# Kernel tuning notes

Measured on AMD Instinct MI355X. Metric: run time of the kernel, lower is better.

## Reference

```python
import jax, jax.numpy as jnp
import numpy as np

N_NODES = 50000
N_EDGES = 1_600_000
D_IN = 256
D_OUT = 256
BATCH = 4


def setup_inputs() -> dict:
    key = jax.random.key(0)
    k1, k2, k3, k4, k5, k6 = jax.random.split(key, 6)
    batch_input = jax.random.normal(k1, (BATCH, N_NODES, D_IN), dtype=jnp.float32)
    adj_rows = jax.random.randint(k2, (N_EDGES,), 0, N_NODES, dtype=jnp.int32)
    adj_cols = jax.random.randint(k3, (N_EDGES,), 0, N_NODES, dtype=jnp.int32)
    adj_vals = jax.random.uniform(k4, (N_EDGES,), dtype=jnp.float32)
    stdv = 1.0 / np.sqrt(D_OUT)
    weight = jax.random.uniform(k5, (D_IN, D_OUT), dtype=jnp.float32, minval=-stdv, maxval=stdv)
    b = jax.random.uniform(k6, (D_OUT,), dtype=jnp.float32, minval=-stdv, maxval=stdv)
    return {"batch_input": batch_input, "adj_rows": adj_rows, "adj_cols": adj_cols,
            "adj_vals": adj_vals, "weight": weight, "b": b}


def reference(batch_input, adj_rows, adj_cols, adj_vals, weight, b):
    # dense projection: [B, N, D_in] @ [D_in, D_out]
    support = jnp.einsum('bnf,fo->bno', batch_input, weight)

    # spmm with COO adjacency: out[r] = sum_e vals[e] * support[cols[e]] for rows[e]==r
    def spmm(s):  # s: [N, D_out]
        msgs = adj_vals[:, None] * s[adj_cols]          # [E, D_out]
        return jax.ops.segment_sum(msgs, adj_rows, num_segments=N_NODES)

    out = jax.vmap(spmm)(support)                       # [B, N, D_out]
    return out + b
```

## Files before the change

### kernel.cpp

```cpp
#include <hip/hip_runtime.h>

#define N_NODES 50000
#define D_DIM   256
#define N_BATCH 4
#define M_TOTAL (N_BATCH * N_NODES)

typedef __attribute__((ext_vector_type(8))) short bf16x8;
typedef __attribute__((ext_vector_type(4))) float f32x4;

__device__ inline float4 fma4(float a, float4 b, float4 c) {
    c.x = fmaf(a, b.x, c.x);
    c.y = fmaf(a, b.y, c.y);
    c.z = fmaf(a, b.z, c.z);
    c.w = fmaf(a, b.w, c.w);
    return c;
}

__device__ inline unsigned short f2bf(float f) {
    unsigned u = __float_as_uint(f);
    u = (u + 0x7fffu + ((u >> 16) & 1u)) >> 16;
    return (unsigned short)u;
}

__device__ inline float4 bf4tof4(ushort4 v) {
    return make_float4(__uint_as_float((unsigned)v.x << 16),
                       __uint_as_float((unsigned)v.y << 16),
                       __uint_as_float((unsigned)v.z << 16),
                       __uint_as_float((unsigned)v.w << 16));
}

__device__ inline int2 nt_edge(const int2* p) {
    long long raw = __builtin_nontemporal_load((const long long*)p);
    int2 r;
    r.x = (int)(unsigned long long)raw;
    r.y = (int)((unsigned long long)raw >> 32);
    return r;
}

__device__ inline void async_copy16(const unsigned short* g, unsigned short* l) {
    __builtin_amdgcn_global_load_lds(
        (const __attribute__((address_space(1))) char*)g,
        (__attribute__((address_space(3))) char*)l, 16, 0, 0);
}

__global__ void zero_kernel(int* __restrict__ p, int n) {
    int i = blockIdx.x * 256 + threadIdx.x;
    if (i < n) p[i] = 0;
}

__global__ void hist_kernel(const int* __restrict__ rows, int* __restrict__ counts, int E) {
    int e = blockIdx.x * 256 + threadIdx.x;
    if (e < E) atomicAdd(&counts[rows[e]], 1);
}

__global__ void scan_kernel(const int* __restrict__ counts, int* __restrict__ starts,
                            int* __restrict__ cursor, int n) {
    __shared__ int wsum[16];
    __shared__ int btot;
    const int tid  = threadIdx.x;
    const int lane = tid & 63;
    const int wid  = tid >> 6;
    int carry = 0;
    for (int base = 0; base < n; base += 1024) {
        int i = base + tid;
        int v = (i < n) ? counts[i] : 0;
        int x = v;
        #pragma unroll
        for (int s = 1; s < 64; s <<= 1) {
            int y = __shfl_up(x, s, 64);
            if (lane >= s) x += y;
        }
        if (lane == 63) wsum[wid] = x;
        __syncthreads();
        if (wid == 0 && lane < 16) {
            int w  = wsum[lane];
            int xx = w;
            #pragma unroll
            for (int s = 1; s < 16; s <<= 1) {
                int y = __shfl_up(xx, s, 64);
                if (lane >= s) xx += y;
            }
            wsum[lane] = xx - w;
            if (lane == 15) btot = xx;
        }
        __syncthreads();
        int excl = carry + wsum[wid] + x - v;
        if (i < n) { starts[i] = excl; cursor[i] = excl; }
        carry += btot;
        __syncthreads();
    }
    if (tid == 0) starts[n] = carry;
}

__global__ void scatter_kernel(const int* __restrict__ rows, const int* __restrict__ cols,
                               const float* __restrict__ vals, int* __restrict__ cursor,
                               int2* __restrict__ csr, int E) {
    int e = blockIdx.x * 256 + threadIdx.x;
    if (e < E) {
        int r   = rows[e];
        int pos = atomicAdd(&cursor[r], 1);
        csr[pos] = make_int2(cols[e], __float_as_int(vals[e]));
    }
}

__global__ void cast_x_kernel(const float4* __restrict__ X, ushort4* __restrict__ Xb, int n4) {
    int i = blockIdx.x * 256 + threadIdx.x;
    if (i < n4) {
        f32x4 v = __builtin_nontemporal_load((const f32x4*)&X[i]);
        ushort4 o;
        o.x = f2bf(v.x); o.y = f2bf(v.y); o.z = f2bf(v.z); o.w = f2bf(v.w);
        Xb[i] = o;
    }
}

__global__ void cast_wt_kernel(const float* __restrict__ W, unsigned short* __restrict__ Wt) {
    int i = blockIdx.x * 256 + threadIdx.x;
    int n = i >> 8, k = i & 255;
    Wt[n * 256 + k] = f2bf(W[k * 256 + n]);
}

__global__ __launch_bounds__(256) void gemm_mfma_kernel(const unsigned short* __restrict__ Xb,
                                                        const unsigned short* __restrict__ Wt,
                                                        unsigned short* __restrict__ sup) {
    __shared__ unsigned short at[128 * 32];
    __shared__ unsigned short bt[128 * 32];
    const int tid  = threadIdx.x;
    const int lane = tid & 63;
    const int wid  = tid >> 6;
    const int wm   = wid & 1, wn = wid >> 1;
    const int row0 = (blockIdx.x >> 1) * 128;
    const int col0 = (blockIdx.x & 1) * 128;
    const int fr    = lane & 15;
    const int fk    = (lane >> 4) * 8;
    const int srow  = lane >> 2;
    const int skoff = (lane & 3) * 8;

    f32x4 acc[4][4];
    #pragma unroll
    for (int a = 0; a < 4; ++a)
        #pragma unroll
        for (int b = 0; b < 4; ++b) acc[a][b] = (f32x4){0.f, 0.f, 0.f, 0.f};

    for (int kc = 0; kc < 256; kc += 32) {
        #pragma unroll
        for (int c = 0; c < 2; ++c) {
            int r = wid * 32 + c * 16;
            int gra = row0 + r + srow; if (gra >= M_TOTAL) gra = M_TOTAL - 1;
            async_copy16(Xb + (size_t)gra * 256 + kc + skoff, &at[r * 32]);
            int grb = col0 + r + srow;
            async_copy16(Wt + (size_t)grb * 256 + kc + skoff, &bt[r * 32]);
        }
        __syncthreads();
        bf16x8 af[4], bfr[4];
        #pragma unroll
        for (int t = 0; t < 4; ++t) {
            af[t]  = *(const bf16x8*)&at[(wm * 64 + t * 16 + fr) * 32 + fk];
            bfr[t] = *(const bf16x8*)&bt[(wn * 64 + t * 16 + fr) * 32 + fk];
        }
        #pragma unroll
        for (int tn = 0; tn < 4; ++tn)
            #pragma unroll
            for (int tm = 0; tm < 4; ++tm)
                acc[tn][tm] = __builtin_amdgcn_mfma_f32_16x16x32_bf16(bfr[tn], af[tm], acc[tn][tm], 0, 0, 0);
        __syncthreads();
    }

    #pragma unroll
    for (int tm = 0; tm < 4; ++tm) {
        int gr = row0 + wm * 64 + tm * 16 + fr;
        if (gr < M_TOTAL) {
            int b    = (int)((unsigned)gr / (unsigned)N_NODES);
            int node = gr - b * N_NODES;
            size_t base = ((size_t)node * 4 + b) * 256;
            #pragma unroll
            for (int tn = 0; tn < 4; ++tn) {
                int col = col0 + wn * 64 + tn * 16 + (lane >> 4) * 4;
                ushort4 o;
                o.x = f2bf(acc[tn][tm][0]);
                o.y = f2bf(acc[tn][tm][1]);
                o.z = f2bf(acc[tn][tm][2]);
                o.w = f2bf(acc[tn][tm][3]);
                *(ushort4*)&sup[base + col] = o;
            }
        }
    }
}

__global__ __launch_bounds__(256) void spmm_kernel(const unsigned short* __restrict__ sup,
                                                   const int* __restrict__ starts,
                                                   const int2* __restrict__ csr,
                                                   const float* __restrict__ bias,
                                                   float* __restrict__ out) {
    const int row  = blockIdx.x;
    const int b    = threadIdx.x >> 6;
    const int lane = threadIdx.x & 63;
    const unsigned short* supb = sup + (size_t)b * 256 + (size_t)lane * 4;
    const int s = starts[row];
    const int e = starts[row + 1];
    float4 acc = make_float4(0.f, 0.f, 0.f, 0.f);
    int i = s;
    for (; i + 7 < e; i += 8) {
        int2 ed[8];
        #pragma unroll
        for (int u = 0; u < 8; ++u) ed[u] = nt_edge(&csr[i + u]);
        ushort4 v[8];
        #pragma unroll
        for (int u = 0; u < 8; ++u) v[u] = *(const ushort4*)(supb + (size_t)ed[u].x * 1024);
        #pragma unroll
        for (int u = 0; u < 8; ++u) acc = fma4(__int_as_float(ed[u].y), bf4tof4(v[u]), acc);
    }
    for (; i + 1 < e; i += 2) {
        int2 e0 = nt_edge(&csr[i]);
        int2 e1 = nt_edge(&csr[i + 1]);
        ushort4 v0 = *(const ushort4*)(supb + (size_t)e0.x * 1024);
        ushort4 v1 = *(const ushort4*)(supb + (size_t)e1.x * 1024);
        acc = fma4(__int_as_float(e0.y), bf4tof4(v0), acc);
        acc = fma4(__int_as_float(e1.y), bf4tof4(v1), acc);
    }
    for (; i < e; ++i) {
        int2 e0 = nt_edge(&csr[i]);
        ushort4 v0 = *(const ushort4*)(supb + (size_t)e0.x * 1024);
        acc = fma4(__int_as_float(e0.y), bf4tof4(v0), acc);
    }
    float4 bb = ((const float4*)bias)[lane];
    f32x4 o;
    o.x = acc.x + bb.x; o.y = acc.y + bb.y; o.z = acc.z + bb.z; o.w = acc.w + bb.w;
    f32x4* dst = (f32x4*)out + ((size_t)b * N_NODES + row) * (D_DIM / 4) + lane;
    __builtin_nontemporal_store(o, dst);
}

extern "C" void kernel_launch(void* const* d_in, const int* in_sizes, int n_in,
                              void* d_out, int out_size, void* d_ws, size_t ws_size,
                              hipStream_t stream) {
    const float* X    = (const float*)d_in[0];
    const int*   rows = (const int*)d_in[1];
    const int*   cols = (const int*)d_in[2];
    const float* vals = (const float*)d_in[3];
    const float* W    = (const float*)d_in[4];
    const float* bias = (const float*)d_in[5];
    float*       out  = (float*)d_out;
    const int E = in_sizes[1];

    char* wsb = (char*)d_ws;
    size_t o = 0;
    auto alloc = [&](size_t bytes) -> char* {
        char* p = wsb + o;
        o += (bytes + 255) & ~(size_t)255;
        return p;
    };
    int*  counts = (int*)alloc((size_t)N_NODES * 4);
    int*  starts = (int*)alloc((size_t)(N_NODES + 1) * 4);
    int*  cursor = (int*)alloc((size_t)N_NODES * 4);
    int2* csr    = (int2*)alloc((size_t)E * 8);
    unsigned short* Xb  = (unsigned short*)alloc((size_t)M_TOTAL * D_DIM * 2);
    unsigned short* sup = (unsigned short*)alloc((size_t)N_NODES * N_BATCH * D_DIM * 2);
    unsigned short* Wt  = (unsigned short*)cursor;

    zero_kernel<<<(N_NODES + 255) / 256, 256, 0, stream>>>(counts, N_NODES);
    hist_kernel<<<(E + 255) / 256, 256, 0, stream>>>(rows, counts, E);
    scan_kernel<<<1, 1024, 0, stream>>>(counts, starts, cursor, N_NODES);
    scatter_kernel<<<(E + 255) / 256, 256, 0, stream>>>(rows, cols, vals, cursor, csr, E);

    const int n4 = M_TOTAL * D_DIM / 4;
    cast_x_kernel<<<(n4 + 255) / 256, 256, 0, stream>>>((const float4*)X, (ushort4*)Xb, n4);
    cast_wt_kernel<<<(256 * 256) / 256, 256, 0, stream>>>(W, Wt);

    const int rowTiles = (M_TOTAL + 127) / 128;
    gemm_mfma_kernel<<<rowTiles * 2, 256, 0, stream>>>(Xb, Wt, sup);

    spmm_kernel<<<N_NODES, 256, 0, stream>>>(sup, starts, csr, bias, out);
}
```

Measured before the change: 1.061 ms.

## Fuse X cast into GEMM, parallelize scan, merge init kernels, drop nontemporal edge loads

```diff
diff --git a/kernel.cpp b/kernel.cpp
--- a/kernel.cpp
+++ b/kernel.cpp
@@ -29,23 +29,18 @@
                        __uint_as_float((unsigned)v.w << 16));
 }
 
-__device__ inline int2 nt_edge(const int2* p) {
-    long long raw = __builtin_nontemporal_load((const long long*)p);
-    int2 r;
-    r.x = (int)(unsigned long long)raw;
-    r.y = (int)((unsigned long long)raw >> 32);
-    return r;
-}
-
 __device__ inline void async_copy16(const unsigned short* g, unsigned short* l) {
     __builtin_amdgcn_global_load_lds(
         (const __attribute__((address_space(1))) char*)g,
         (__attribute__((address_space(3))) char*)l, 16, 0, 0);
 }
 
-__global__ void zero_kernel(int* __restrict__ p, int n) {
+__global__ void init_kernel(int* __restrict__ counts, const float* __restrict__ W,
+                            unsigned short* __restrict__ Wt) {
     int i = blockIdx.x * 256 + threadIdx.x;
-    if (i < n) p[i] = 0;
+    if (i < N_NODES) counts[i] = 0;
+    int n = i >> 8, k = i & 255;
+    Wt[n * 256 + k] = f2bf(W[k * 256 + n]);
 }
 
 __global__ void hist_kernel(const int* __restrict__ rows, int* __restrict__ counts, int E) {
@@ -53,43 +48,61 @@
     if (e < E) atomicAdd(&counts[rows[e]], 1);
 }
 
-__global__ void scan_kernel(const int* __restrict__ counts, int* __restrict__ starts,
-                            int* __restrict__ cursor, int n) {
+__global__ __launch_bounds__(1024) void scan1_kernel(const int* __restrict__ counts,
+                                                     int* __restrict__ starts,
+                                                     int* __restrict__ bsum, int n) {
     __shared__ int wsum[16];
     __shared__ int btot;
     const int tid  = threadIdx.x;
     const int lane = tid & 63;
     const int wid  = tid >> 6;
-    int carry = 0;
-    for (int base = 0; base < n; base += 1024) {
-        int i = base + tid;
-        int v = (i < n) ? counts[i] : 0;
-        int x = v;
-        #pragma unroll
-        for (int s = 1; s < 64; s <<= 1) {
-            int y = __shfl_up(x, s, 64);
-            if (lane >= s) x += y;
-        }
-        if (lane == 63) wsum[wid] = x;
-        __syncthreads();
-        if (wid == 0 && lane < 16) {
-            int w  = wsum[lane];
-            int xx = w;
-            #pragma unroll
-            for (int s = 1; s < 16; s <<= 1) {
-                int y = __shfl_up(xx, s, 64);
-                if (lane >= s) xx += y;
-            }
-            wsum[lane] = xx - w;
-            if (lane == 15) btot = xx;
-        }
-        __syncthreads();
-        int excl = carry + wsum[wid] + x - v;
-        if (i < n) { starts[i] = excl; cursor[i] = excl; }
-        carry += btot;
-        __syncthreads();
-    }
-    if (tid == 0) starts[n] = carry;
+    int i = blockIdx.x * 1024 + tid;
+    int v = (i < n) ? counts[i] : 0;
+    int x = v;
+    #pragma unroll
+    for (int s = 1; s < 64; s <<= 1) {
+        int y = __shfl_up(x, s, 64);
+        if (lane >= s) x += y;
+    }
+    if (lane == 63) wsum[wid] = x;
+    __syncthreads();
+    if (wid == 0 && lane < 16) {
+        int w  = wsum[lane];
+        int xx = w;
+        #pragma unroll
+        for (int s = 1; s < 16; s <<= 1) {
+            int y = __shfl_up(xx, s, 64);
+            if (lane >= s) xx += y;
+        }
+        wsum[lane] = xx - w;
+        if (lane == 15) btot = xx;
+    }
+    __syncthreads();
+    if (i < n) starts[i] = wsum[wid] + x - v;
+    if (tid == 0) bsum[blockIdx.x] = btot;
+}
+
+__global__ void scan2_kernel(int* __restrict__ bsum, int* __restrict__ starts, int nb, int n) {
+    int lane = threadIdx.x;
+    int v = (lane < nb) ? bsum[lane] : 0;
+    int x = v;
+    #pragma unroll
+    for (int s = 1; s < 64; s <<= 1) {
+        int y = __shfl_up(x, s, 64);
+        if (lane >= s) x += y;
+    }
+    if (lane < nb) bsum[lane] = x - v;
+    if (lane == 63) starts[n] = x;
+}
+
+__global__ void scan3_kernel(int* __restrict__ starts, int* __restrict__ cursor,
+                             const int* __restrict__ bsum, int n) {
+    int i = blockIdx.x * 256 + threadIdx.x;
+    if (i < n) {
+        int s = starts[i] + bsum[i >> 10];
+        starts[i] = s;
+        cursor[i] = s;
+    }
 }
 
 __global__ void scatter_kernel(const int* __restrict__ rows, const int* __restrict__ cols,
@@ -103,23 +116,7 @@
     }
 }
 
-__global__ void cast_x_kernel(const float4* __restrict__ X, ushort4* __restrict__ Xb, int n4) {
-    int i = blockIdx.x * 256 + threadIdx.x;
-    if (i < n4) {
-        f32x4 v = __builtin_nontemporal_load((const f32x4*)&X[i]);
-        ushort4 o;
-        o.x = f2bf(v.x); o.y = f2bf(v.y); o.z = f2bf(v.z); o.w = f2bf(v.w);
-        Xb[i] = o;
-    }
-}
-
-__global__ void cast_wt_kernel(const float* __restrict__ W, unsigned short* __restrict__ Wt) {
-    int i = blockIdx.x * 256 + threadIdx.x;
-    int n = i >> 8, k = i & 255;
-    Wt[n * 256 + k] = f2bf(W[k * 256 + n]);
-}
-
-__global__ __launch_bounds__(256) void gemm_mfma_kernel(const unsigned short* __restrict__ Xb,
+__global__ __launch_bounds__(256) void gemm_mfma_kernel(const float* __restrict__ X,
                                                         const unsigned short* __restrict__ Wt,
                                                         unsigned short* __restrict__ sup) {
     __shared__ unsigned short at[128 * 32];
@@ -145,10 +142,23 @@
         #pragma unroll
         for (int c = 0; c < 2; ++c) {
             int r = wid * 32 + c * 16;
-            int gra = row0 + r + srow; if (gra >= M_TOTAL) gra = M_TOTAL - 1;
-            async_copy16(Xb + (size_t)gra * 256 + kc + skoff, &at[r * 32]);
             int grb = col0 + r + srow;
             async_copy16(Wt + (size_t)grb * 256 + kc + skoff, &bt[r * 32]);
+        }
+        #pragma unroll
+        for (int s0 = 0; s0 < 2; ++s0) {
+            int s    = tid + s0 * 256;
+            int arow = s >> 2;
+            int koff = (s & 3) * 8;
+            int gra  = row0 + arow; if (gra >= M_TOTAL) gra = M_TOTAL - 1;
+            const float* src = X + (size_t)gra * 256 + kc + koff;
+            float4 v0 = *(const float4*)src;
+            float4 v1 = *(const float4*)(src + 4);
+            ushort4 lo, hi;
+            lo.x = f2bf(v0.x); lo.y = f2bf(v0.y); lo.z = f2bf(v0.z); lo.w = f2bf(v0.w);
+            hi.x = f2bf(v1.x); hi.y = f2bf(v1.y); hi.z = f2bf(v1.z); hi.w = f2bf(v1.w);
+            *(ushort4*)&at[arow * 32 + koff]     = lo;
+            *(ushort4*)&at[arow * 32 + koff + 4] = hi;
         }
         __syncthreads();
         bf16x8 af[4], bfr[4];
@@ -202,7 +212,7 @@
     for (; i + 7 < e; i += 8) {
         int2 ed[8];
         #pragma unroll
-        for (int u = 0; u < 8; ++u) ed[u] = nt_edge(&csr[i + u]);
+        for (int u = 0; u < 8; ++u) ed[u] = csr[i + u];
         ushort4 v[8];
         #pragma unroll
         for (int u = 0; u < 8; ++u) v[u] = *(const ushort4*)(supb + (size_t)ed[u].x * 1024);
@@ -210,15 +220,15 @@
         for (int u = 0; u < 8; ++u) acc = fma4(__int_as_float(ed[u].y), bf4tof4(v[u]), acc);
     }
     for (; i + 1 < e; i += 2) {
-        int2 e0 = nt_edge(&csr[i]);
-        int2 e1 = nt_edge(&csr[i + 1]);
+        int2 e0 = csr[i];
+        int2 e1 = csr[i + 1];
         ushort4 v0 = *(const ushort4*)(supb + (size_t)e0.x * 1024);
         ushort4 v1 = *(const ushort4*)(supb + (size_t)e1.x * 1024);
         acc = fma4(__int_as_float(e0.y), bf4tof4(v0), acc);
         acc = fma4(__int_as_float(e1.y), bf4tof4(v1), acc);
     }
     for (; i < e; ++i) {
-        int2 e0 = nt_edge(&csr[i]);
+        int2 e0 = csr[i];
         ushort4 v0 = *(const ushort4*)(supb + (size_t)e0.x * 1024);
         acc = fma4(__int_as_float(e0.y), bf4tof4(v0), acc);
     }
@@ -251,22 +261,24 @@
     int*  counts = (int*)alloc((size_t)N_NODES * 4);
     int*  starts = (int*)alloc((size_t)(N_NODES + 1) * 4);
     int*  cursor = (int*)alloc((size_t)N_NODES * 4);
+    int*  bsum   = (int*)alloc(64 * 4);
+    unsigned short* Wt = (unsigned short*)alloc((size_t)256 * 256 * 2);
     int2* csr    = (int2*)alloc((size_t)E * 8);
-    unsigned short* Xb  = (unsigned short*)alloc((size_t)M_TOTAL * D_DIM * 2);
     unsigned short* sup = (unsigned short*)alloc((size_t)N_NODES * N_BATCH * D_DIM * 2);
-    unsigned short* Wt  = (unsigned short*)cursor;
-
-    zero_kernel<<<(N_NODES + 255) / 256, 256, 0, stream>>>(counts, N_NODES);
+
+    const int NB = (N_NODES + 1023) / 1024;
+
+    init_kernel<<<256, 256, 0, stream>>>(counts, W, Wt);
     hist_kernel<<<(E + 255) / 256, 256, 0, stream>>>(rows, counts, E);
-    scan_kernel<<<1, 1024, 0, stream>>>(counts, starts, cursor, N_NODES);
+
+    scan1_kernel<<<NB, 1024, 0, stream>>>(counts, starts, bsum, N_NODES);
+    scan2_kernel<<<1, 64, 0, stream>>>(bsum, starts, NB, N_NODES);
+    scan3_kernel<<<(N_NODES + 255) / 256, 256, 0, stream>>>(starts, cursor, bsum, N_NODES);
+
     scatter_kernel<<<(E + 255) / 256, 256, 0, stream>>>(rows, cols, vals, cursor, csr, E);
 
-    const int n4 = M_TOTAL * D_DIM / 4;
-    cast_x_kernel<<<(n4 + 255) / 256, 256, 0, stream>>>((const float4*)X, (ushort4*)Xb, n4);
-    cast_wt_kernel<<<(256 * 256) / 256, 256, 0, stream>>>(W, Wt);
-
     const int rowTiles = (M_TOTAL + 127) / 128;
-    gemm_mfma_kernel<<<rowTiles * 2, 256, 0, stream>>>(Xb, Wt, sup);
+    gemm_mfma_kernel<<<rowTiles * 2, 256, 0, stream>>>(X, Wt, sup);
 
     spmm_kernel<<<N_NODES, 256, 0, stream>>>(sup, starts, csr, bias, out);
 }
```

Result: faster. 1.007 ms (-5.2%).
